# Optimization experiments

Measured on AMD Instinct MI355X. Metric: run time of the kernel, lower is better.

The kernel has to match this reference:

```python
import jax, jax.numpy as jnp
import numpy as np

B, NIMG, H, W, C = 4, 4, 80, 80, 256
NH = 8
C1 = C // 8          # 32
CPH = C1 // NH       # 4 per-head conv channels
K2D = 4              # deformable attention sampling points
HD2 = C1 // NH       # 4 head dim for 2D deformable attention
INNER = 32           # 3D deformable attention inner dim
DSF = (2, 8, 8)
OSC = jnp.array([2.0, 8.0, 8.0], jnp.float32)


def _bilin2d(img, px, py):
    # img [B,C,H,W]; px,py [B,K] pixel coords -> [B,K,C], zero-padded outside
    Bb, Cc, Hh, Ww = img.shape
    x0 = jnp.floor(px); y0 = jnp.floor(py)
    wx = px - x0; wy = py - y0
    bidx = jnp.arange(Bb)[:, None]
    def g(yy, xx):
        valid = (xx >= 0) & (xx <= Ww - 1) & (yy >= 0) & (yy <= Hh - 1)
        xi = jnp.clip(xx, 0, Ww - 1).astype(jnp.int32)
        yi = jnp.clip(yy, 0, Hh - 1).astype(jnp.int32)
        return img[bidx, :, yi, xi] * valid[..., None]
    return (g(y0, x0) * ((1 - wy) * (1 - wx))[..., None]
          + g(y0, x0 + 1) * ((1 - wy) * wx)[..., None]
          + g(y0 + 1, x0) * (wy * (1 - wx))[..., None]
          + g(y0 + 1, x0 + 1) * (wy * wx)[..., None])


def _trilin(img, z, y, x):
    # img [B,C,D,H,W]; z,y,x [B,K] -> [B,K,C]
    Bb, Cc, Dd, Hh, Ww = img.shape
    z0 = jnp.floor(z); y0 = jnp.floor(y); x0 = jnp.floor(x)
    wz = z - z0; wy = y - y0; wx = x - x0
    bidx = jnp.arange(Bb)[:, None]
    def g(zz, yy, xx):
        valid = (zz >= 0) & (zz <= Dd - 1) & (yy >= 0) & (yy <= Hh - 1) & (xx >= 0) & (xx <= Ww - 1)
        zi = jnp.clip(zz, 0, Dd - 1).astype(jnp.int32)
        yi = jnp.clip(yy, 0, Hh - 1).astype(jnp.int32)
        xi = jnp.clip(xx, 0, Ww - 1).astype(jnp.int32)
        return img[bidx, :, zi, yi, xi] * valid[..., None]
    out = 0.
    for dz in (0., 1.):
        for dy in (0., 1.):
            for dx in (0., 1.):
                w = ((1 - wz) if dz == 0. else wz) * ((1 - wy) if dy == 0. else wy) * ((1 - wx) if dx == 0. else wx)
                out = out + g(z0 + dz, y0 + dy, x0 + dx) * w[..., None]
    return out


def _fwd(x, W_qkv, b_qkv, W_fc, b_fc, W_doff, b_doff, W_dep, b_dep, W_st, b_st,
         W_off2d, b_off2d, W_attw, b_attw, W_val, b_val, W_out2d, b_out2d,
         W_q3, b_q3, W_k3, b_k3, W_v3, b_v3, W_offA, b_offA, W_offB, b_offB,
         W_out3, b_out3, rate1, rate2, nimg):
    xb = jnp.transpose(x, (1, 0, 2))                       # [B, nHW, C]
    Bb = xb.shape[0]
    qkv = xb @ W_qkv + b_qkv                               # [B, nHW, 2*C1]
    # ---------- deformable-conv (ACMix) branch ----------
    f_all = qkv.reshape(Bb, nimg * H * W, 2 * NH, CPH).transpose(0, 2, 1, 3)
    f9 = jnp.einsum('oc,bcnk->bonk', W_fc, f_all) + b_fc[None, :, None, None]
    f_conv = f9.transpose(0, 3, 1, 2).reshape(Bb, 9 * CPH, nimg, H, W)
    fin = f_conv.transpose(0, 2, 1, 3, 4).reshape(Bb * nimg, 9 * CPH, H, W)
    off = jax.lax.conv_general_dilated(fin, W_doff, (1, 1), ((1, 1), (1, 1)),
          dimension_numbers=('NCHW', 'OIHW', 'NCHW')) + b_doff[None, :, None, None]
    off = off.reshape(Bb * nimg, 9, 2, H, W)               # (dy,dx) per 3x3 tap
    hh, ww = jnp.meshgrid(jnp.arange(H, dtype=jnp.float32), jnp.arange(W, dtype=jnp.float32), indexing='ij')
    tap = jnp.arange(9)
    ky = (tap // 3 - 1).astype(jnp.float32); kx = (tap % 3 - 1).astype(jnp.float32)
    py = hh[None, None] + ky[None, :, None, None] + off[:, :, 0]
    px = ww[None, None] + kx[None, :, None, None] + off[:, :, 1]
    samp = _bilin2d(fin, px.reshape(Bb * nimg, -1), py.reshape(Bb * nimg, -1))
    samp = samp.reshape(Bb * nimg, 9, H, W, 9 * CPH).transpose(0, 4, 1, 2, 3)
    sg = samp.reshape(Bb * nimg, CPH, 9, 9, H, W)          # [Bn, g, cin_pg, taps, H, W]
    wg = W_dep.reshape(CPH, 27, 9, 9)                      # [g, out_pg, cin_pg, taps]
    dep = jnp.einsum('bgikhw,goik->bgohw', sg, wg).reshape(Bb * nimg, 27 * CPH, H, W) + b_dep[None, :, None, None]
    oc = dep.reshape(Bb, nimg, 27 * CPH, H, W).transpose(0, 2, 1, 3, 4)
    st_in = oc.reshape(Bb, CPH, 27, nimg, H, W)
    st = jnp.einsum('bginhw,goi->bgonhw', st_in, W_st).reshape(Bb, C, nimg, H, W) + b_st[None, :, None, None, None]
    out_conv = st.transpose(2, 3, 4, 0, 1).reshape(nimg * H * W, Bb, C)
    # ---------- per-frame 2D deformable attention ----------
    qk = qkv.reshape(Bb, nimg, H, W, 2, C1)
    q2 = qk[..., 0, :].reshape(Bb * nimg, H, W, C1)
    k2 = qk[..., 1, :].reshape(Bb * nimg, H, W, C1)
    gy, gx = jnp.meshgrid(jnp.arange(H, dtype=jnp.float32) / (H - 1),
                          jnp.arange(W, dtype=jnp.float32) / (W - 1), indexing='ij')
    ref = jnp.stack([gx, gy], -1)                          # [H,W,2] normalized (x,y)
    off2 = (q2 @ W_off2d + b_off2d).reshape(Bb * nimg, H, W, NH, K2D, 2)
    attw = jax.nn.softmax((q2 @ W_attw + b_attw).reshape(Bb * nimg, H, W, NH, K2D), axis=-1)
    v2 = (k2 @ W_val + b_val).reshape(Bb * nimg, H, W, NH, HD2)
    vimg = v2.transpose(0, 3, 4, 1, 2).reshape(Bb * nimg * NH, HD2, H, W)
    loc = ref[None, :, :, None, None, :] + off2 / jnp.array([W, H], jnp.float32)
    ppx = (loc[..., 0] * (W - 1)).transpose(0, 3, 1, 2, 4).reshape(Bb * nimg * NH, H * W * K2D)
    ppy = (loc[..., 1] * (H - 1)).transpose(0, 3, 1, 2, 4).reshape(Bb * nimg * NH, H * W * K2D)
    s2 = _bilin2d(vimg, ppx, ppy).reshape(Bb * nimg, NH, H, W, K2D, HD2)
    a2 = jnp.einsum('bhwnk,bnhwkd->bhwnd', attw, s2).reshape(Bb * nimg, H, W, C1)
    a2 = (a2 @ W_out2d + b_out2d).reshape(Bb, nimg, H, W, C1)
    # faithful reproduction of the source's frame-concat bug: frames [0,0,1,...,nimg-2]
    idx = jnp.array([0] + list(range(nimg - 1)))
    x3 = a2[:, idx].transpose(0, 4, 1, 2, 3)               # [B, C1, nimg, H, W]
    # ---------- 3D deformable attention ----------
    q3 = jnp.einsum('oc,bcnhw->bonhw', W_q3, x3) + b_q3[None, :, None, None, None]
    hid = jax.lax.conv_general_dilated(q3, W_offA, DSF, ((1, 1), (1, 1), (1, 1)),
          dimension_numbers=('NCDHW', 'OIDHW', 'NCDHW')) + b_offA[None, :, None, None, None]
    hid = jax.nn.gelu(hid)
    off3 = jnp.einsum('oc,bcnhw->bonhw', W_offB, hid) + b_offB[None, :, None, None, None]
    off3 = jnp.tanh(off3) * OSC[None, :, None, None, None]
    npr, hpr, wpr = off3.shape[2], off3.shape[3], off3.shape[4]
    gz, gy2, gx2 = jnp.meshgrid(jnp.arange(npr, dtype=jnp.float32) * 2 + 0.5,
                                jnp.arange(hpr, dtype=jnp.float32) * 8 + 3.5,
                                jnp.arange(wpr, dtype=jnp.float32) * 8 + 3.5, indexing='ij')
    cz = (gz[None] + off3[:, 0]).reshape(Bb, -1)
    cy = (gy2[None] + off3[:, 1]).reshape(Bb, -1)
    cx = (gx2[None] + off3[:, 2]).reshape(Bb, -1)
    kf = jnp.einsum('oc,bcnhw->bonhw', W_k3, x3) + b_k3[None, :, None, None, None]
    vf = jnp.einsum('oc,bcnhw->bonhw', W_v3, x3) + b_v3[None, :, None, None, None]
    ks_ = _trilin(kf, cz, cy, cx)                          # [B, L, INNER]
    vs_ = _trilin(vf, cz, cy, cx)
    qf = q3.reshape(Bb, INNER, -1).transpose(0, 2, 1)      # [B, N, INNER]
    at = jax.nn.softmax(jnp.einsum('bnd,bld->bnl', qf, ks_) * (INNER ** -0.5), axis=-1)
    o3 = jnp.einsum('bnl,bld->bnd', at, vs_).transpose(0, 2, 1).reshape(Bb, INNER, nimg, H, W)
    o3 = jnp.einsum('oc,bcnhw->bonhw', W_out3, o3) + b_out3[None, :, None, None, None]
    xattn = o3.transpose(2, 3, 4, 0, 1).reshape(nimg * H * W, Bb, C)
    return rate1 * xattn + rate2 * out_conv


def _p(key, shape, s=0.02):
    return jax.random.normal(key, shape, jnp.float32) * s


def setup_inputs() -> dict:
    key = jax.random.key(0)
    ks = jax.random.split(key, 20)
    z = lambda *s: jnp.zeros(s, jnp.float32)
    return {
        'x': jax.random.normal(ks[0], (NIMG * H * W, B, C), jnp.float32),
        'W_qkv': _p(ks[1], (C, C // 4)), 'b_qkv': z(C // 4),
        'W_fc': _p(ks[2], (9, 2 * NH)), 'b_fc': z(9),
        'W_doff': _p(ks[3], (18, 9 * CPH, 3, 3), 0.01), 'b_doff': z(18),
        'W_dep': _p(ks[4], (27 * CPH, 9, 3, 3)), 'b_dep': z(27 * CPH),
        'W_st': _p(ks[5], (CPH, C // CPH, 27)), 'b_st': z(C),
        'W_off2d': _p(ks[6], (C1, NH * K2D * 2), 0.01), 'b_off2d': z(NH * K2D * 2),
        'W_attw': _p(ks[7], (C1, NH * K2D)), 'b_attw': z(NH * K2D),
        'W_val': _p(ks[8], (C1, C1)), 'b_val': z(C1),
        'W_out2d': _p(ks[9], (C1, C1)), 'b_out2d': z(C1),
        'W_q3': _p(ks[10], (INNER, C1)), 'b_q3': z(INNER),
        'W_k3': _p(ks[11], (INNER, C1)), 'b_k3': z(INNER),
        'W_v3': _p(ks[12], (INNER, C1)), 'b_v3': z(INNER),
        'W_offA': _p(ks[13], (INNER, INNER, 4, 10, 10), 0.01), 'b_offA': z(INNER),
        'W_offB': _p(ks[14], (3, INNER), 0.01), 'b_offB': z(3),
        'W_out3': _p(ks[15], (C, INNER)), 'b_out3': z(C),
        'rate1': jnp.full((1,), 0.5, jnp.float32),
        'rate2': jnp.full((1,), 0.5, jnp.float32),
        'nimg': NIMG,
    }


def reference(x, W_qkv, b_qkv, W_fc, b_fc, W_doff, b_doff, W_dep, b_dep, W_st, b_st,
              W_off2d, b_off2d, W_attw, b_attw, W_val, b_val, W_out2d, b_out2d,
              W_q3, b_q3, W_k3, b_k3, W_v3, b_v3, W_offA, b_offA, W_offB, b_offB,
              W_out3, b_out3, rate1, rate2, nimg):
    return _fwd(x, W_qkv, b_qkv, W_fc, b_fc, W_doff, b_doff, W_dep, b_dep, W_st, b_st,
                W_off2d, b_off2d, W_attw, b_attw, W_val, b_val, W_out2d, b_out2d,
                W_q3, b_q3, W_k3, b_k3, W_v3, b_v3, W_offA, b_offA, W_offB, b_offB,
                W_out3, b_out3, rate1, rate2, nimg)
```

## Files before the change

### kernel.cpp

```cpp
#include <hip/hip_runtime.h>
#include <math.h>

#define B_     4
#define NIMG_  4
#define H_     80
#define W_     80
#define C_     256
#define NH_    8
#define HW_    6400
#define NQ_    25600
#define NPIX_  102400
#define L3_    200

#define WS_QKV 0u
#define WS_Q3  0u
#define WS_KF  3276800u
#define WS_FIN 6553600u
#define WS_A2  6553600u
#define WS_O3  6553600u
#define WS_OFF 10240000u
#define WS_CRD 10240000u
#define WS_KS  10242400u
#define WS_VS  10268000u
#define WS_V2  12083200u
#define WS_VF  12083200u

__global__ __launch_bounds__(256) void k_qkv(const float* __restrict__ x,
        const float* __restrict__ Wq, const float* __restrict__ bq,
        float* __restrict__ qkv) {
    __shared__ __align__(16) float xs[32][256];
    int t = threadIdx.x;
    int row0 = blockIdx.x * 32;
    for (int it = 0; it < 8; ++it) {
        int idx = t + it * 256;
        int r = idx >> 6;
        int f4 = idx & 63;
        int row = row0 + r;
        int b = row / NQ_, n = row % NQ_;
        const float4* src = (const float4*)(x + ((size_t)n * B_ + b) * C_);
        ((float4*)&xs[r][0])[f4] = src[f4];
    }
    __syncthreads();
    int j = t & 63;
    int rbase = (t >> 6) * 8;
    float acc[8];
    #pragma unroll
    for (int r = 0; r < 8; ++r) acc[r] = 0.f;
    for (int c4 = 0; c4 < 64; ++c4) {
        float w0 = Wq[(c4 * 4 + 0) * 64 + j];
        float w1 = Wq[(c4 * 4 + 1) * 64 + j];
        float w2 = Wq[(c4 * 4 + 2) * 64 + j];
        float w3 = Wq[(c4 * 4 + 3) * 64 + j];
        #pragma unroll
        for (int r = 0; r < 8; ++r) {
            float4 xv = ((const float4*)&xs[rbase + r][0])[c4];
            acc[r] += xv.x * w0 + xv.y * w1 + xv.z * w2 + xv.w * w3;
        }
    }
    float bias = bq[j];
    #pragma unroll
    for (int r = 0; r < 8; ++r) {
        int row = row0 + rbase + r;
        qkv[(size_t)row * 64 + j] = acc[r] + bias;
    }
}

__global__ __launch_bounds__(256) void k_fin_v2(const float* __restrict__ qkv,
        const float* __restrict__ Wfc, const float* __restrict__ bfc,
        const float* __restrict__ Wval, const float* __restrict__ bval,
        float* __restrict__ fin, float* __restrict__ v2) {
    __shared__ float WvalL[1024], WfcL[144], bfcL[9], bvalL[32];
    int t = threadIdx.x;
    for (int d = t; d < 1024; d += 256) WvalL[d] = Wval[d];
    if (t < 144) WfcL[t] = Wfc[t];
    if (t >= 160 && t < 169) bfcL[t - 160] = bfc[t - 160];
    if (t >= 192 && t < 224) bvalL[t - 192] = bval[t - 192];
    __syncthreads();
    int P = blockIdx.x * 256 + t;
    int b = P / NQ_, nq = P % NQ_;
    int n = nq / HW_, hw = nq % HW_;
    int bn = b * NIMG_ + n;
    float q[64];
    const float4* qp = (const float4*)(qkv + (size_t)P * 64);
    #pragma unroll
    for (int i = 0; i < 16; ++i) ((float4*)q)[i] = qp[i];
    float fo[36];
    #pragma unroll
    for (int k = 0; k < 4; ++k)
        #pragma unroll
        for (int o = 0; o < 9; ++o) fo[k * 9 + o] = bfcL[o];
    for (int c = 0; c < 16; ++c) {
        #pragma unroll
        for (int o = 0; o < 9; ++o) {
            float wv = WfcL[o * 16 + c];
            #pragma unroll
            for (int k = 0; k < 4; ++k) fo[k * 9 + o] += wv * q[c * 4 + k];
        }
    }
    float* fp = fin + ((size_t)bn * HW_ + hw) * 36;
    #pragma unroll
    for (int i = 0; i < 9; ++i) ((float4*)fp)[i] = ((float4*)fo)[i];
    float vo[32];
    #pragma unroll
    for (int j = 0; j < 32; ++j) vo[j] = bvalL[j];
    for (int c = 0; c < 32; ++c) {
        float qc = q[32 + c];
        #pragma unroll
        for (int j = 0; j < 32; ++j) vo[j] += qc * WvalL[c * 32 + j];
    }
    float* vp = v2 + ((size_t)bn * HW_ + hw) * 32;
    #pragma unroll
    for (int i = 0; i < 8; ++i) ((float4*)vp)[i] = ((float4*)vo)[i];
}

__global__ __launch_bounds__(256) void k_offconv(const float* __restrict__ fin,
        const float* __restrict__ Wdoff, const float* __restrict__ bdoff,
        float* __restrict__ off) {
    __shared__ float Wl[5832];
    int t = threadIdx.x;
    for (int d = t; d < 5832; d += 256) {
        int tap = d / 648, r = d % 648, c = r / 18, o = r % 18;
        Wl[d] = Wdoff[(o * 36 + c) * 9 + tap];
    }
    __syncthreads();
    int P = blockIdx.x * 256 + t;
    int bn = P / HW_, hw = P % HW_;
    int h = hw / W_, w = hw % W_;
    float acc[18];
    #pragma unroll
    for (int o = 0; o < 18; ++o) acc[o] = bdoff[o];
    for (int ky = 0; ky < 3; ++ky) {
        int hh = h + ky - 1;
        if (hh < 0 || hh >= H_) continue;
        for (int kx = 0; kx < 3; ++kx) {
            int ww = w + kx - 1;
            if (ww < 0 || ww >= W_) continue;
            const float* base = fin + ((size_t)bn * HW_ + hh * W_ + ww) * 36;
            const float* wl = Wl + (ky * 3 + kx) * 648;
            #pragma unroll
            for (int c4 = 0; c4 < 9; ++c4) {
                float4 v = ((const float4*)base)[c4];
                const float* w0 = wl + (c4 * 4) * 18;
                #pragma unroll
                for (int o = 0; o < 18; ++o)
                    acc[o] += v.x * w0[o] + v.y * w0[18 + o] + v.z * w0[36 + o] + v.w * w0[54 + o];
            }
        }
    }
    float* op = off + (size_t)P * 18;
    #pragma unroll
    for (int o = 0; o < 18; ++o) op[o] = acc[o];
}

__global__ __launch_bounds__(512, 4) void k_depst(const float* __restrict__ fin,
        const float* __restrict__ off, const float* __restrict__ Wdep,
        const float* __restrict__ bdep, const float* __restrict__ Wst,
        const float* __restrict__ bst, const float* __restrict__ rate2p,
        float* __restrict__ out) {
    __shared__ __align__(16) float wdepL[9072];
    __shared__ __align__(16) float wstL[6944];
    __shared__ float offL[2304];
    __shared__ float bdepL[108];
    __shared__ float bstL[256];
    int t = threadIdx.x;
    int bx = blockIdx.x;
    int pb = (bx & 7) * 100 + (bx >> 3);
    int P0 = pb * 128;
    for (int d = t; d < 9072; d += 512) {
        int g2 = d / 2268, r = d % 2268;
        int k = r / 252, r2 = r % 252;
        int i = r2 / 28, o = r2 % 28;
        wdepL[d] = (o < 27) ? Wdep[(size_t)(g2 * 27 + o) * 81 + i * 9 + k] : 0.f;
    }
    for (int d = t; d < 6944; d += 512) {
        int g2 = d / 1736, r = d % 1736;
        int i = r >> 6, o = r & 63;
        wstL[d] = (r < 1728) ? Wst[g2 * 1728 + o * 27 + i] : 0.f;
    }
    for (int d = t; d < 2304; d += 512) offL[d] = off[(size_t)P0 * 18 + d];
    if (t < 108) bdepL[t] = bdep[t];
    if (t < 256) bstL[t] = bst[t];
    __syncthreads();
    int g = t & 3, ploc = t >> 2;
    int P = P0 + ploc;
    int bn = P / HW_, hw = P % HW_;
    int h = hw / W_, w = hw % W_;
    int b = bn >> 2, n = bn & 3;
    const float* finb = fin + (size_t)bn * HW_ * 36 + g * 9;
    const float* wdg = wdepL + g * 2268;
    const float* wsg = wstL + g * 1736;
    float acc[27];
    #pragma unroll
    for (int o = 0; o < 27; ++o) acc[o] = 0.f;
    float hf = (float)h, wf = (float)w;
    #pragma unroll 1
    for (int k = 0; k < 9; ++k) {
        float py = hf + (float)(k / 3 - 1) + offL[ploc * 18 + k * 2 + 0];
        float px = wf + (float)(k % 3 - 1) + offL[ploc * 18 + k * 2 + 1];
        float y0f = floorf(py), x0f = floorf(px);
        float wy = py - y0f, wx = px - x0f;
        float wy0 = 1.f - wy, wx0 = 1.f - wx;
        float vy0 = (y0f >= 0.f && y0f <= 79.f) ? 1.f : 0.f;
        float vy1 = (y0f >= -1.f && y0f <= 78.f) ? 1.f : 0.f;
        float vx0 = (x0f >= 0.f && x0f <= 79.f) ? 1.f : 0.f;
        float vx1 = (x0f >= -1.f && x0f <= 78.f) ? 1.f : 0.f;
        int yi0 = (int)fminf(fmaxf(y0f, 0.f), 79.f);
        int yi1 = (int)fminf(fmaxf(y0f + 1.f, 0.f), 79.f);
        int xi0 = (int)fminf(fmaxf(x0f, 0.f), 79.f);
        int xi1 = (int)fminf(fmaxf(x0f + 1.f, 0.f), 79.f);
        float w00 = wy0 * wx0 * vy0 * vx0;
        float w01 = wy0 * wx  * vy0 * vx1;
        float w10 = wy  * wx0 * vy1 * vx0;
        float w11 = wy  * wx  * vy1 * vx1;
        const float* c00 = finb + ((size_t)(yi0 * W_ + xi0)) * 36;
        const float* c01 = finb + ((size_t)(yi0 * W_ + xi1)) * 36;
        const float* c10 = finb + ((size_t)(yi1 * W_ + xi0)) * 36;
        const float* c11 = finb + ((size_t)(yi1 * W_ + xi1)) * 36;
        float s[9];
        #pragma unroll
        for (int i = 0; i < 9; ++i)
            s[i] = w00 * c00[i] + w01 * c01[i] + w10 * c10[i] + w11 * c11[i];
        const float* wk = wdg + k * 252;
        #pragma unroll
        for (int i = 0; i < 9; ++i) {
            float si = s[i];
            const float4* rw = (const float4*)(wk + i * 28);
            float4 q0 = rw[0], q1 = rw[1], q2 = rw[2], q3 = rw[3];
            float4 q4 = rw[4], q5 = rw[5], q6 = rw[6];
            acc[0]  += si * q0.x; acc[1]  += si * q0.y; acc[2]  += si * q0.z; acc[3]  += si * q0.w;
            acc[4]  += si * q1.x; acc[5]  += si * q1.y; acc[6]  += si * q1.z; acc[7]  += si * q1.w;
            acc[8]  += si * q2.x; acc[9]  += si * q2.y; acc[10] += si * q2.z; acc[11] += si * q2.w;
            acc[12] += si * q3.x; acc[13] += si * q3.y; acc[14] += si * q3.z; acc[15] += si * q3.w;
            acc[16] += si * q4.x; acc[17] += si * q4.y; acc[18] += si * q4.z; acc[19] += si * q4.w;
            acc[20] += si * q5.x; acc[21] += si * q5.y; acc[22] += si * q5.z; acc[23] += si * q5.w;
            acc[24] += si * q6.x; acc[25] += si * q6.y; acc[26] += si * q6.z;
        }
    }
    #pragma unroll
    for (int i = 0; i < 27; ++i) acc[i] += bdepL[g * 27 + i];
    float r2v = rate2p[0];
    float* ob = out + ((size_t)(n * HW_ + hw) * B_ + b) * C_ + g * 64;
    #pragma unroll 1
    for (int half = 0; half < 2; ++half) {
        float ro[32];
        #pragma unroll
        for (int o = 0; o < 32; ++o) ro[o] = bstL[g * 64 + half * 32 + o];
        #pragma unroll
        for (int i = 0; i < 27; ++i) {
            float ai = acc[i];
            const float4* rw = (const float4*)(wsg + i * 64 + half * 32);
            #pragma unroll
            for (int j = 0; j < 8; ++j) {
                float4 wv = rw[j];
                ro[j * 4 + 0] += ai * wv.x;
                ro[j * 4 + 1] += ai * wv.y;
                ro[j * 4 + 2] += ai * wv.z;
                ro[j * 4 + 3] += ai * wv.w;
            }
        }
        float4* obv = (float4*)(ob + half * 32);
        #pragma unroll
        for (int o4 = 0; o4 < 8; ++o4)
            obv[o4] = make_float4(r2v * ro[o4 * 4 + 0], r2v * ro[o4 * 4 + 1],
                                  r2v * ro[o4 * 4 + 2], r2v * ro[o4 * 4 + 3]);
    }
}

__global__ __launch_bounds__(256) void k_attn2d(const float* __restrict__ qkv,
        const float* __restrict__ v2,
        const float* __restrict__ Woff, const float* __restrict__ boff,
        const float* __restrict__ Watt, const float* __restrict__ batt,
        const float* __restrict__ Wout, const float* __restrict__ bout,
        float* __restrict__ a2) {
    __shared__ float WoffL[2048], WattL[1024], WoutL[1024];
    __shared__ float boffL[64], battL[32], boutL[32];
    int t = threadIdx.x;
    for (int d = t; d < 2048; d += 256) WoffL[d] = Woff[d];
    for (int d = t; d < 1024; d += 256) { WattL[d] = Watt[d]; WoutL[d] = Wout[d]; }
    if (t < 64) boffL[t] = boff[t];
    else if (t < 96) battL[t - 64] = batt[t - 64];
    else if (t < 128) boutL[t - 96] = bout[t - 96];
    __syncthreads();
    int P = blockIdx.x * 256 + t;
    int b = P / NQ_, nq = P % NQ_;
    int n = nq / HW_, hw = nq % HW_;
    int h = hw / W_, w = hw % W_;
    int bn = b * NIMG_ + n;
    float q[32];
    const float4* qp = (const float4*)(qkv + (size_t)P * 64);
    #pragma unroll
    for (int i = 0; i < 8; ++i) ((float4*)q)[i] = qp[i];
    const float* vbase = v2 + (size_t)bn * HW_ * 32;
    float a2v[32];
    #pragma unroll
    for (int i = 0; i < 32; ++i) a2v[i] = 0.f;
    for (int nh = 0; nh < 8; ++nh) {
        float t0 = battL[nh * 4 + 0], t1 = battL[nh * 4 + 1];
        float t2 = battL[nh * 4 + 2], t3 = battL[nh * 4 + 3];
        for (int c = 0; c < 32; ++c) {
            float qc = q[c];
            const float* wr = WattL + c * 32 + nh * 4;
            t0 += qc * wr[0]; t1 += qc * wr[1]; t2 += qc * wr[2]; t3 += qc * wr[3];
        }
        float m = fmaxf(fmaxf(t0, t1), fmaxf(t2, t3));
        float e0 = expf(t0 - m), e1 = expf(t1 - m), e2 = expf(t2 - m), e3 = expf(t3 - m);
        float inv = 1.f / (e0 + e1 + e2 + e3);
        float pk[4] = {e0 * inv, e1 * inv, e2 * inv, e3 * inv};
        #pragma unroll
        for (int kk = 0; kk < 4; ++kk) {
            int j0 = nh * 8 + kk * 2;
            float ox = boffL[j0], oy = boffL[j0 + 1];
            for (int c = 0; c < 32; ++c) {
                float qc = q[c];
                ox += qc * WoffL[c * 64 + j0];
                oy += qc * WoffL[c * 64 + j0 + 1];
            }
            float ppx = (float)w + ox * (79.f / 80.f);
            float ppy = (float)h + oy * (79.f / 80.f);
            float x0 = floorf(ppx), y0 = floorf(ppy);
            float wx = ppx - x0, wy = ppy - y0;
            float s0 = 0.f, s1 = 0.f, s2 = 0.f, s3 = 0.f;
            #pragma unroll
            for (int cy = 0; cy < 2; ++cy) {
                float yf = y0 + (float)cy;
                if (yf < 0.f || yf > 79.f) continue;
                float wyf = cy ? wy : 1.f - wy;
                int yi = (int)yf;
                #pragma unroll
                for (int cx = 0; cx < 2; ++cx) {
                    float xf = x0 + (float)cx;
                    if (xf < 0.f || xf > 79.f) continue;
                    float wgt = wyf * (cx ? wx : 1.f - wx);
                    int xi = (int)xf;
                    float4 vv = *(const float4*)(vbase + ((size_t)yi * W_ + xi) * 32 + nh * 4);
                    s0 += wgt * vv.x; s1 += wgt * vv.y; s2 += wgt * vv.z; s3 += wgt * vv.w;
                }
            }
            float p = pk[kk];
            a2v[nh * 4 + 0] += p * s0; a2v[nh * 4 + 1] += p * s1;
            a2v[nh * 4 + 2] += p * s2; a2v[nh * 4 + 3] += p * s3;
        }
    }
    float ro[32];
    #pragma unroll
    for (int o = 0; o < 32; ++o) ro[o] = boutL[o];
    for (int c = 0; c < 32; ++c) {
        float ac = a2v[c];
        const float* wr = WoutL + c * 32;
        #pragma unroll
        for (int o = 0; o < 32; ++o) ro[o] += ac * wr[o];
    }
    float* op = a2 + ((size_t)bn * HW_ + hw) * 32;
    #pragma unroll
    for (int i = 0; i < 8; ++i) ((float4*)op)[i] = ((float4*)ro)[i];
}

__global__ __launch_bounds__(256) void k_qkv3(const float* __restrict__ a2,
        const float* __restrict__ Wq3, const float* __restrict__ bq3,
        const float* __restrict__ Wk3, const float* __restrict__ bk3,
        const float* __restrict__ Wv3, const float* __restrict__ bv3,
        float* __restrict__ q3, float* __restrict__ kf, float* __restrict__ vf) {
    __shared__ float Wq3L[1024], Wk3L[1024], Wv3L[1024];
    __shared__ float bq3L[32], bk3L[32], bv3L[32];
    int t = threadIdx.x;
    for (int d = t; d < 1024; d += 256) {
        Wq3L[d] = Wq3[d]; Wk3L[d] = Wk3[d]; Wv3L[d] = Wv3[d];
    }
    if (t < 32) { bq3L[t] = bq3[t]; bk3L[t] = bk3[t]; bv3L[t] = bv3[t]; }
    __syncthreads();
    int idx = blockIdx.x * 256 + t;
    int bn = idx / HW_, hw = idx % HW_;
    int b = bn >> 2, n = bn & 3;
    int ns = (n == 0) ? 0 : n - 1;
    const float* src = a2 + ((size_t)(b * 4 + ns) * HW_ + hw) * 32;
    float v[32];
    #pragma unroll
    for (int i = 0; i < 8; ++i) ((float4*)v)[i] = ((const float4*)src)[i];
    float oq[32], ok[32], ov[32];
    #pragma unroll
    for (int o = 0; o < 32; ++o) {
        float aq = bq3L[o], ak = bk3L[o], av = bv3L[o];
        #pragma unroll
        for (int c = 0; c < 32; ++c) {
            aq += Wq3L[o * 32 + c] * v[c];
            ak += Wk3L[o * 32 + c] * v[c];
            av += Wv3L[o * 32 + c] * v[c];
        }
        oq[o] = aq; ok[o] = ak; ov[o] = av;
    }
    float* qo = q3 + (size_t)idx * 32;
    float* ko = kf + (size_t)idx * 32;
    float* vo = vf + (size_t)idx * 32;
    #pragma unroll
    for (int i = 0; i < 8; ++i) {
        ((float4*)qo)[i] = ((float4*)oq)[i];
        ((float4*)ko)[i] = ((float4*)ok)[i];
        ((float4*)vo)[i] = ((float4*)ov)[i];
    }
}

__global__ __launch_bounds__(256) void k_offs3d(const float* __restrict__ q3,
        const float* __restrict__ WoffA, const float* __restrict__ boffA,
        const float* __restrict__ WoffB, const float* __restrict__ boffB,
        float* __restrict__ coords) {
    __shared__ float red[4][128];
    __shared__ float hidl[128];
    int t = threadIdx.x;
    int blk = blockIdx.x;
    int zo = blk / 100, r = blk % 100, ho = r / 10, wo = r % 10;
    float acc[4][32];
    #pragma unroll
    for (int b = 0; b < 4; ++b)
        #pragma unroll
        for (int o = 0; o < 32; ++o) acc[b][o] = 0.f;
    for (int tap = t; tap < 400; tap += 256) {
        int kz = tap / 100, r2 = tap % 100, ky = r2 / 10, kx = r2 % 10;
        int zi = zo * 2 + kz - 1, hi = ho * 8 + ky - 1, wi = wo * 8 + kx - 1;
        if (zi < 0 || zi >= NIMG_ || hi < 0 || hi >= H_ || wi < 0 || wi >= W_) continue;
        const float* wb = WoffA + tap;
        int sp = hi * W_ + wi;
        for (int c = 0; c < 32; ++c) {
            float vb[4];
            #pragma unroll
            for (int b = 0; b < 4; ++b)
                vb[b] = q3[((size_t)(b * 4 + zi) * HW_ + sp) * 32 + c];
            #pragma unroll
            for (int o = 0; o < 32; ++o) {
                float wv = wb[(o * 32 + c) * 400];
                #pragma unroll
                for (int b = 0; b < 4; ++b) acc[b][o] += vb[b] * wv;
            }
        }
    }
    #pragma unroll
    for (int b = 0; b < 4; ++b)
        #pragma unroll
        for (int o = 0; o < 32; ++o)
            for (int sh = 32; sh >= 1; sh >>= 1)
                acc[b][o] += __shfl_xor(acc[b][o], sh);
    int lane = t & 63, wv = t >> 6;
    if (lane == 0)
        for (int b = 0; b < 4; ++b)
            for (int o = 0; o < 32; ++o) red[wv][b * 32 + o] = acc[b][o];
    __syncthreads();
    if (t < 128) {
        float v = red[0][t] + red[1][t] + red[2][t] + red[3][t] + boffA[t & 31];
        float v3 = v * v * v;
        hidl[t] = 0.5f * v * (1.f + tanhf(0.7978845608028654f * (v + 0.044715f * v3)));
    }
    __syncthreads();
    if (t < 12) {
        int b = t / 3, j = t % 3;
        float a = boffB[j];
        for (int o = 0; o < 32; ++o) a += WoffB[j * 32 + o] * hidl[b * 32 + o];
        float osc = (j == 0) ? 2.f : 8.f;
        float base = (j == 0) ? (zo * 2 + 0.5f) : ((j == 1) ? (ho * 8 + 3.5f) : (wo * 8 + 3.5f));
        coords[((size_t)b * L3_ + blk) * 3 + j] = base + tanhf(a) * osc;
    }
}

__global__ __launch_bounds__(256) void k_trisample(const float* __restrict__ kf,
        const float* __restrict__ vf, const float* __restrict__ coords,
        float* __restrict__ ks, float* __restrict__ vs) {
    int t = threadIdx.x;
    int wv = blockIdx.x * 4 + (t >> 6);
    int b = wv / L3_, l = wv % L3_;
    int lane = t & 63;
    int c = lane & 31;
    const float* src = (lane < 32) ? kf : vf;
    float* dst = (lane < 32) ? ks : vs;
    const float* cp = coords + ((size_t)b * L3_ + l) * 3;
    float cz = cp[0], cy = cp[1], cx = cp[2];
    float z0 = floorf(cz), y0 = floorf(cy), x0 = floorf(cx);
    float wz = cz - z0, wy = cy - y0, wx = cx - x0;
    float acc = 0.f;
    #pragma unroll
    for (int dz = 0; dz < 2; ++dz) {
        float zf = z0 + (float)dz;
        if (zf < 0.f || zf > 3.f) continue;
        float wzf = dz ? wz : 1.f - wz;
        int zi = (int)zf;
        #pragma unroll
        for (int dy = 0; dy < 2; ++dy) {
            float yf = y0 + (float)dy;
            if (yf < 0.f || yf > 79.f) continue;
            float wyf = wzf * (dy ? wy : 1.f - wy);
            int yi = (int)yf;
            #pragma unroll
            for (int dx = 0; dx < 2; ++dx) {
                float xf = x0 + (float)dx;
                if (xf < 0.f || xf > 79.f) continue;
                float wgt = wyf * (dx ? wx : 1.f - wx);
                int xi = (int)xf;
                acc += wgt * src[((size_t)(b * 4 + zi) * HW_ + yi * W_ + xi) * 32 + c];
            }
        }
    }
    dst[((size_t)b * L3_ + l) * 32 + c] = acc;
}

__global__ __launch_bounds__(256) void k_attn3d(const float* __restrict__ q3,
        const float* __restrict__ ks, const float* __restrict__ vs,
        float* __restrict__ o3) {
    __shared__ __align__(16) float ksl[L3_ * 32];
    __shared__ __align__(16) float vsl[L3_ * 32];
    int t = threadIdx.x;
    int b = blockIdx.x / 100;
    int chunk = blockIdx.x % 100;
    const float4* ksg = (const float4*)(ks + (size_t)b * L3_ * 32);
    const float4* vsg = (const float4*)(vs + (size_t)b * L3_ * 32);
    for (int d = t; d < L3_ * 8; d += 256) {
        ((float4*)ksl)[d] = ksg[d];
        ((float4*)vsl)[d] = vsg[d];
    }
    __syncthreads();
    int N = chunk * 256 + t;
    float q[32];
    const float4* qp = (const float4*)(q3 + ((size_t)b * NQ_ + N) * 32);
    #pragma unroll
    for (int i = 0; i < 8; ++i) ((float4*)q)[i] = qp[i];
    const float scale = 0.17677669529663687f;
    float den = 0.f;
    float o[32];
    #pragma unroll
    for (int c = 0; c < 32; ++c) o[c] = 0.f;
    for (int l = 0; l < L3_; ++l) {
        const float4* kp = (const float4*)(ksl + l * 32);
        float s = 0.f;
        #pragma unroll
        for (int c4 = 0; c4 < 8; ++c4) {
            float4 kv = kp[c4];
            s += q[c4 * 4 + 0] * kv.x + q[c4 * 4 + 1] * kv.y + q[c4 * 4 + 2] * kv.z + q[c4 * 4 + 3] * kv.w;
        }
        float p = expf(s * scale);
        den += p;
        const float4* vp = (const float4*)(vsl + l * 32);
        #pragma unroll
        for (int c4 = 0; c4 < 8; ++c4) {
            float4 vv = vp[c4];
            o[c4 * 4 + 0] += p * vv.x; o[c4 * 4 + 1] += p * vv.y;
            o[c4 * 4 + 2] += p * vv.z; o[c4 * 4 + 3] += p * vv.w;
        }
    }
    float inv = 1.f / den;
    float* op = o3 + ((size_t)b * NQ_ + N) * 32;
    #pragma unroll
    for (int c = 0; c < 32; ++c) op[c] = o[c] * inv;
}

__global__ __launch_bounds__(256) void k_final(const float* __restrict__ o3,
        const float* __restrict__ W, const float* __restrict__ bias,
        const float* __restrict__ r1p, float* __restrict__ out) {
    __shared__ float o3T[32 * 128];
    __shared__ float WT[32 * 260];
    int t = threadIdx.x;
    int R0 = blockIdx.x * 128;
    {
        int row = t >> 1, k0 = (t & 1) * 16;
        int R = R0 + row;
        int b = R & 3, N = R >> 2;
        const float* src = o3 + ((size_t)b * NQ_ + N) * 32 + k0;
        #pragma unroll
        for (int j = 0; j < 16; ++j) o3T[(k0 + j) * 128 + row] = src[j];
    }
    for (int d = t; d < 8192; d += 256) {
        int c = d >> 5, k = d & 31;
        WT[k * 260 + c] = W[d];
    }
    __syncthreads();
    int tc = t & 15;
    int tr = t >> 4;
    int r0 = tr * 8;
    float acc[8][16];
    #pragma unroll
    for (int i = 0; i < 8; ++i)
        #pragma unroll
        for (int j = 0; j < 16; ++j) acc[i][j] = 0.f;
    #pragma unroll 1
    for (int k = 0; k < 32; ++k) {
        float a[8];
        *(float4*)&a[0] = *(const float4*)&o3T[k * 128 + r0];
        *(float4*)&a[4] = *(const float4*)&o3T[k * 128 + r0 + 4];
        float wv[16];
        #pragma unroll
        for (int ci = 0; ci < 16; ++ci) wv[ci] = WT[k * 260 + tc + 16 * ci];
        #pragma unroll
        for (int i = 0; i < 8; ++i)
            #pragma unroll
            for (int j = 0; j < 16; ++j) acc[i][j] += a[i] * wv[j];
    }
    float r1 = r1p[0];
    float bs[16];
    #pragma unroll
    for (int ci = 0; ci < 16; ++ci) bs[ci] = bias[tc + 16 * ci];
    #pragma unroll 1
    for (int i = 0; i < 8; ++i) {
        size_t rowbase = (size_t)(R0 + r0 + i) * 256;
        #pragma unroll
        for (int j = 0; j < 16; ++j) {
            size_t oi = rowbase + tc + 16 * j;
            out[oi] = r1 * (acc[i][j] + bs[j]) + out[oi];
        }
    }
}

extern "C" void kernel_launch(void* const* d_in, const int* in_sizes, int n_in,
                              void* d_out, int out_size, void* d_ws, size_t ws_size,
                              hipStream_t stream) {
    (void)in_sizes; (void)n_in; (void)out_size; (void)ws_size;
    const float* x      = (const float*)d_in[0];
    const float* W_qkv  = (const float*)d_in[1];
    const float* b_qkv  = (const float*)d_in[2];
    const float* W_fc   = (const float*)d_in[3];
    const float* b_fc   = (const float*)d_in[4];
    const float* W_doff = (const float*)d_in[5];
    const float* b_doff = (const float*)d_in[6];
    const float* W_dep  = (const float*)d_in[7];
    const float* b_dep  = (const float*)d_in[8];
    const float* W_st   = (const float*)d_in[9];
    const float* b_st   = (const float*)d_in[10];
    const float* W_off2d= (const float*)d_in[11];
    const float* b_off2d= (const float*)d_in[12];
    const float* W_attw = (const float*)d_in[13];
    const float* b_attw = (const float*)d_in[14];
    const float* W_val  = (const float*)d_in[15];
    const float* b_val  = (const float*)d_in[16];
    const float* W_out2d= (const float*)d_in[17];
    const float* b_out2d= (const float*)d_in[18];
    const float* W_q3   = (const float*)d_in[19];
    const float* b_q3   = (const float*)d_in[20];
    const float* W_k3   = (const float*)d_in[21];
    const float* b_k3   = (const float*)d_in[22];
    const float* W_v3   = (const float*)d_in[23];
    const float* b_v3   = (const float*)d_in[24];
    const float* W_offA = (const float*)d_in[25];
    const float* b_offA = (const float*)d_in[26];
    const float* W_offB = (const float*)d_in[27];
    const float* b_offB = (const float*)d_in[28];
    const float* W_out3 = (const float*)d_in[29];
    const float* b_out3 = (const float*)d_in[30];
    const float* rate1  = (const float*)d_in[31];
    const float* rate2  = (const float*)d_in[32];

    float* ws  = (float*)d_ws;
    float* out = (float*)d_out;
    float* qkv = ws + WS_QKV;
    float* fin = ws + WS_FIN;
    float* off = ws + WS_OFF;
    float* v2  = ws + WS_V2;
    float* a2  = ws + WS_A2;
    float* q3  = ws + WS_Q3;
    float* kf  = ws + WS_KF;
    float* vf  = ws + WS_VF;
    float* crd = ws + WS_CRD;
    float* ks  = ws + WS_KS;
    float* vs  = ws + WS_VS;
    float* o3w = ws + WS_O3;

    k_qkv      <<<3200,   256, 0, stream>>>(x, W_qkv, b_qkv, qkv);
    k_fin_v2   <<<400,    256, 0, stream>>>(qkv, W_fc, b_fc, W_val, b_val, fin, v2);
    k_offconv  <<<400,    256, 0, stream>>>(fin, W_doff, b_doff, off);
    k_depst    <<<800,    512, 0, stream>>>(fin, off, W_dep, b_dep, W_st, b_st, rate2, out);
    k_attn2d   <<<400,    256, 0, stream>>>(qkv, v2, W_off2d, b_off2d, W_attw, b_attw, W_out2d, b_out2d, a2);
    k_qkv3     <<<400,    256, 0, stream>>>(a2, W_q3, b_q3, W_k3, b_k3, W_v3, b_v3, q3, kf, vf);
    k_offs3d   <<<200,    256, 0, stream>>>(q3, W_offA, b_offA, W_offB, b_offB, crd);
    k_trisample<<<200,    256, 0, stream>>>(kf, vf, crd, ks, vs);
    k_attn3d   <<<400,    256, 0, stream>>>(q3, ks, vs, o3w);
    k_final    <<<800,    256, 0, stream>>>(o3w, W_out3, b_out3, rate1, out);
}
```

Measured before the change: 918.2 us.

## Split fin into per-group padded planes and give each depst block one group

The 36-channel fin buffer becomes four group-major planes, each holding 9 values per pixel padded to 12. The deformable-conv kernel now gives one group per block of 256 threads, so each block loads only that group's weights into LDS, which shrinks shared memory and raises occupancy. Offsets are now read straight from global memory instead of being staged in LDS, and bilinear taps use aligned float4 loads. The qkv output is split into separate q and k buffers and the workspace layout is reshuffled, at the cost of more padded bytes and a different access pattern in offconv.

```diff
diff --git a/kernel.cpp b/kernel.cpp
--- a/kernel.cpp
+++ b/kernel.cpp
@@ -12,22 +12,23 @@
 #define NPIX_  102400
 #define L3_    200
 
-#define WS_QKV 0u
-#define WS_Q3  0u
-#define WS_KF  3276800u
-#define WS_FIN 6553600u
-#define WS_A2  6553600u
-#define WS_O3  6553600u
-#define WS_OFF 10240000u
-#define WS_CRD 10240000u
-#define WS_KS  10242400u
-#define WS_VS  10268000u
-#define WS_V2  12083200u
-#define WS_VF  12083200u
+#define WS_QH   0u
+#define WS_KH   3276800u
+#define WS_V2   6553600u
+#define WS_FING 9830400u
+#define WS_OFF  3276800u
+#define WS_A2   9830400u
+#define WS_Q3   0u
+#define WS_KF   3276800u
+#define WS_VF   6553600u
+#define WS_CRD  9830400u
+#define WS_KS   9832800u
+#define WS_VS   9858400u
+#define WS_O3   3276800u
 
 __global__ __launch_bounds__(256) void k_qkv(const float* __restrict__ x,
         const float* __restrict__ Wq, const float* __restrict__ bq,
-        float* __restrict__ qkv) {
+        float* __restrict__ qh, float* __restrict__ kh) {
     __shared__ __align__(16) float xs[32][256];
     int t = threadIdx.x;
     int row0 = blockIdx.x * 32;
@@ -61,14 +62,17 @@
     #pragma unroll
     for (int r = 0; r < 8; ++r) {
         int row = row0 + rbase + r;
-        qkv[(size_t)row * 64 + j] = acc[r] + bias;
-    }
-}
-
-__global__ __launch_bounds__(256) void k_fin_v2(const float* __restrict__ qkv,
+        float vres = acc[r] + bias;
+        if (j < 32) qh[(size_t)row * 32 + j] = vres;
+        else        kh[(size_t)row * 32 + (j - 32)] = vres;
+    }
+}
+
+__global__ __launch_bounds__(256) void k_fin_v2(const float* __restrict__ qh,
+        const float* __restrict__ kh,
         const float* __restrict__ Wfc, const float* __restrict__ bfc,
         const float* __restrict__ Wval, const float* __restrict__ bval,
-        float* __restrict__ fin, float* __restrict__ v2) {
+        float* __restrict__ fing, float* __restrict__ v2) {
     __shared__ float WvalL[1024], WfcL[144], bfcL[9], bvalL[32];
     int t = threadIdx.x;
     for (int d = t; d < 1024; d += 256) WvalL[d] = Wval[d];
@@ -81,9 +85,12 @@
     int n = nq / HW_, hw = nq % HW_;
     int bn = b * NIMG_ + n;
     float q[64];
-    const float4* qp = (const float4*)(qkv + (size_t)P * 64);
-    #pragma unroll
-    for (int i = 0; i < 16; ++i) ((float4*)q)[i] = qp[i];
+    const float4* qp = (const float4*)(qh + (size_t)P * 32);
+    const float4* kp = (const float4*)(kh + (size_t)P * 32);
+    #pragma unroll
+    for (int i = 0; i < 8; ++i) ((float4*)q)[i] = qp[i];
+    #pragma unroll
+    for (int i = 0; i < 8; ++i) ((float4*)q)[8 + i] = kp[i];
     float fo[36];
     #pragma unroll
     for (int k = 0; k < 4; ++k)
@@ -97,9 +104,13 @@
             for (int k = 0; k < 4; ++k) fo[k * 9 + o] += wv * q[c * 4 + k];
         }
     }
-    float* fp = fin + ((size_t)bn * HW_ + hw) * 36;
-    #pragma unroll
-    for (int i = 0; i < 9; ++i) ((float4*)fp)[i] = ((float4*)fo)[i];
+    #pragma unroll
+    for (int g = 0; g < 4; ++g) {
+        float* fp = fing + ((size_t)(g * 16 + bn) * HW_ + hw) * 12;
+        ((float4*)fp)[0] = make_float4(fo[g * 9 + 0], fo[g * 9 + 1], fo[g * 9 + 2], fo[g * 9 + 3]);
+        ((float4*)fp)[1] = make_float4(fo[g * 9 + 4], fo[g * 9 + 5], fo[g * 9 + 6], fo[g * 9 + 7]);
+        ((float4*)fp)[2] = make_float4(fo[g * 9 + 8], 0.f, 0.f, 0.f);
+    }
     float vo[32];
     #pragma unroll
     for (int j = 0; j < 32; ++j) vo[j] = bvalL[j];
@@ -113,7 +124,7 @@
     for (int i = 0; i < 8; ++i) ((float4*)vp)[i] = ((float4*)vo)[i];
 }
 
-__global__ __launch_bounds__(256) void k_offconv(const float* __restrict__ fin,
+__global__ __launch_bounds__(256) void k_offconv(const float* __restrict__ fing,
         const float* __restrict__ Wdoff, const float* __restrict__ bdoff,
         float* __restrict__ off) {
     __shared__ float Wl[5832];
@@ -135,15 +146,21 @@
         for (int kx = 0; kx < 3; ++kx) {
             int ww = w + kx - 1;
             if (ww < 0 || ww >= W_) continue;
-            const float* base = fin + ((size_t)bn * HW_ + hh * W_ + ww) * 36;
+            int sp = hh * W_ + ww;
             const float* wl = Wl + (ky * 3 + kx) * 648;
             #pragma unroll
-            for (int c4 = 0; c4 < 9; ++c4) {
-                float4 v = ((const float4*)base)[c4];
-                const float* w0 = wl + (c4 * 4) * 18;
+            for (int g = 0; g < 4; ++g) {
+                const float4* base = (const float4*)(fing
+                        + ((size_t)(g * 16 + bn) * HW_ + sp) * 12);
+                float4 p0 = base[0], p1 = base[1], p2 = base[2];
+                float vals[9] = {p0.x, p0.y, p0.z, p0.w, p1.x, p1.y, p1.z, p1.w, p2.x};
                 #pragma unroll
-                for (int o = 0; o < 18; ++o)
-                    acc[o] += v.x * w0[o] + v.y * w0[18 + o] + v.z * w0[36 + o] + v.w * w0[54 + o];
+                for (int idx = 0; idx < 9; ++idx) {
+                    const float* w0 = wl + (g * 9 + idx) * 18;
+                    float vv = vals[idx];
+                    #pragma unroll
+                    for (int o = 0; o < 18; ++o) acc[o] += vv * w0[o];
+                }
             }
         }
     }
@@ -152,51 +169,46 @@
     for (int o = 0; o < 18; ++o) op[o] = acc[o];
 }
 
-__global__ __launch_bounds__(512, 4) void k_depst(const float* __restrict__ fin,
+__global__ __launch_bounds__(256, 6) void k_depst(const float* __restrict__ fing,
         const float* __restrict__ off, const float* __restrict__ Wdep,
         const float* __restrict__ bdep, const float* __restrict__ Wst,
         const float* __restrict__ bst, const float* __restrict__ rate2p,
         float* __restrict__ out) {
-    __shared__ __align__(16) float wdepL[9072];
-    __shared__ __align__(16) float wstL[6944];
-    __shared__ float offL[2304];
-    __shared__ float bdepL[108];
-    __shared__ float bstL[256];
+    __shared__ __align__(16) float wdepL[2268];
+    __shared__ __align__(16) float wstL[1728];
+    __shared__ float bdepL[27];
+    __shared__ float bstL[64];
     int t = threadIdx.x;
     int bx = blockIdx.x;
-    int pb = (bx & 7) * 100 + (bx >> 3);
-    int P0 = pb * 128;
-    for (int d = t; d < 9072; d += 512) {
-        int g2 = d / 2268, r = d % 2268;
-        int k = r / 252, r2 = r % 252;
+    int u = (bx & 7) * 200 + (bx >> 3);
+    int chunk = u >> 2, g = u & 3;
+    for (int d = t; d < 2268; d += 256) {
+        int k = d / 252, r2 = d % 252;
         int i = r2 / 28, o = r2 % 28;
-        wdepL[d] = (o < 27) ? Wdep[(size_t)(g2 * 27 + o) * 81 + i * 9 + k] : 0.f;
-    }
-    for (int d = t; d < 6944; d += 512) {
-        int g2 = d / 1736, r = d % 1736;
-        int i = r >> 6, o = r & 63;
-        wstL[d] = (r < 1728) ? Wst[g2 * 1728 + o * 27 + i] : 0.f;
-    }
-    for (int d = t; d < 2304; d += 512) offL[d] = off[(size_t)P0 * 18 + d];
-    if (t < 108) bdepL[t] = bdep[t];
-    if (t < 256) bstL[t] = bst[t];
-    __syncthreads();
-    int g = t & 3, ploc = t >> 2;
-    int P = P0 + ploc;
+        wdepL[d] = (o < 27) ? Wdep[(size_t)(g * 27 + o) * 81 + i * 9 + k] : 0.f;
+    }
+    for (int d = t; d < 1728; d += 256) {
+        int i = d >> 6, o = d & 63;
+        wstL[d] = Wst[g * 1728 + o * 27 + i];
+    }
+    if (t < 27) bdepL[t] = bdep[g * 27 + t];
+    if (t >= 32 && t < 96) bstL[t - 32] = bst[g * 64 + (t - 32)];
+    __syncthreads();
+    int P = chunk * 256 + t;
     int bn = P / HW_, hw = P % HW_;
     int h = hw / W_, w = hw % W_;
     int b = bn >> 2, n = bn & 3;
-    const float* finb = fin + (size_t)bn * HW_ * 36 + g * 9;
-    const float* wdg = wdepL + g * 2268;
-    const float* wsg = wstL + g * 1736;
+    const float* finb = fing + (size_t)(g * 16 + bn) * (HW_ * 12);
+    const float* offp = off + (size_t)P * 18;
     float acc[27];
     #pragma unroll
     for (int o = 0; o < 27; ++o) acc[o] = 0.f;
     float hf = (float)h, wf = (float)w;
     #pragma unroll 1
     for (int k = 0; k < 9; ++k) {
-        float py = hf + (float)(k / 3 - 1) + offL[ploc * 18 + k * 2 + 0];
-        float px = wf + (float)(k % 3 - 1) + offL[ploc * 18 + k * 2 + 1];
+        float2 od = *(const float2*)(offp + k * 2);
+        float py = hf + (float)(k / 3 - 1) + od.x;
+        float px = wf + (float)(k % 3 - 1) + od.y;
         float y0f = floorf(py), x0f = floorf(px);
         float wy = py - y0f, wx = px - x0f;
         float wy0 = 1.f - wy, wx0 = 1.f - wx;
@@ -212,43 +224,64 @@
         float w01 = wy0 * wx  * vy0 * vx1;
         float w10 = wy  * wx0 * vy1 * vx0;
         float w11 = wy  * wx  * vy1 * vx1;
-        const float* c00 = finb + ((size_t)(yi0 * W_ + xi0)) * 36;
-        const float* c01 = finb + ((size_t)(yi0 * W_ + xi1)) * 36;
-        const float* c10 = finb + ((size_t)(yi1 * W_ + xi0)) * 36;
-        const float* c11 = finb + ((size_t)(yi1 * W_ + xi1)) * 36;
+        const float4* c00 = (const float4*)(finb + (size_t)(yi0 * W_ + xi0) * 12);
+        const float4* c01 = (const float4*)(finb + (size_t)(yi0 * W_ + xi1) * 12);
+        const float4* c10 = (const float4*)(finb + (size_t)(yi1 * W_ + xi0) * 12);
+        const float4* c11 = (const float4*)(finb + (size_t)(yi1 * W_ + xi1) * 12);
         float s[9];
-        #pragma unroll
-        for (int i = 0; i < 9; ++i)
-            s[i] = w00 * c00[i] + w01 * c01[i] + w10 * c10[i] + w11 * c11[i];
-        const float* wk = wdg + k * 252;
+        {
+            float4 p0 = c00[0], p1 = c00[1], p2 = c00[2];
+            s[0] = w00 * p0.x; s[1] = w00 * p0.y; s[2] = w00 * p0.z; s[3] = w00 * p0.w;
+            s[4] = w00 * p1.x; s[5] = w00 * p1.y; s[6] = w00 * p1.z; s[7] = w00 * p1.w;
+            s[8] = w00 * p2.x;
+        }
+        {
+            float4 p0 = c01[0], p1 = c01[1], p2 = c01[2];
+            s[0] += w01 * p0.x; s[1] += w01 * p0.y; s[2] += w01 * p0.z; s[3] += w01 * p0.w;
+            s[4] += w01 * p1.x; s[5] += w01 * p1.y; s[6] += w01 * p1.z; s[7] += w01 * p1.w;
+            s[8] += w01 * p2.x;
+        }
+        {
+            float4 p0 = c10[0], p1 = c10[1], p2 = c10[2];
+            s[0] += w10 * p0.x; s[1] += w10 * p0.y; s[2] += w10 * p0.z; s[3] += w10 * p0.w;
+            s[4] += w10 * p1.x; s[5] += w10 * p1.y; s[6] += w10 * p1.z; s[7] += w10 * p1.w;
+            s[8] += w10 * p2.x;
+        }
+        {
+            float4 p0 = c11[0], p1 = c11[1], p2 = c11[2];
+            s[0] += w11 * p0.x; s[1] += w11 * p0.y; s[2] += w11 * p0.z; s[3] += w11 * p0.w;
+            s[4] += w11 * p1.x; s[5] += w11 * p1.y; s[6] += w11 * p1.z; s[7] += w11 * p1.w;
+            s[8] += w11 * p2.x;
+        }
+        const float* wk = wdepL + k * 252;
         #pragma unroll
         for (int i = 0; i < 9; ++i) {
             float si = s[i];
             const float4* rw = (const float4*)(wk + i * 28);
-            float4 q0 = rw[0], q1 = rw[1], q2 = rw[2], q3 = rw[3];
+            float4 q0 = rw[0], q1 = rw[1], q2 = rw[2], q3v = rw[3];
             float4 q4 = rw[4], q5 = rw[5], q6 = rw[6];
-            acc[0]  += si * q0.x; acc[1]  += si * q0.y; acc[2]  += si * q0.z; acc[3]  += si * q0.w;
-            acc[4]  += si * q1.x; acc[5]  += si * q1.y; acc[6]  += si * q1.z; acc[7]  += si * q1.w;
-            acc[8]  += si * q2.x; acc[9]  += si * q2.y; acc[10] += si * q2.z; acc[11] += si * q2.w;
-            acc[12] += si * q3.x; acc[13] += si * q3.y; acc[14] += si * q3.z; acc[15] += si * q3.w;
-            acc[16] += si * q4.x; acc[17] += si * q4.y; acc[18] += si * q4.z; acc[19] += si * q4.w;
-            acc[20] += si * q5.x; acc[21] += si * q5.y; acc[22] += si * q5.z; acc[23] += si * q5.w;
-            acc[24] += si * q6.x; acc[25] += si * q6.y; acc[26] += si * q6.z;
-        }
-    }
-    #pragma unroll
-    for (int i = 0; i < 27; ++i) acc[i] += bdepL[g * 27 + i];
+            acc[0]  += si * q0.x;  acc[1]  += si * q0.y;  acc[2]  += si * q0.z;  acc[3]  += si * q0.w;
+            acc[4]  += si * q1.x;  acc[5]  += si * q1.y;  acc[6]  += si * q1.z;  acc[7]  += si * q1.w;
+            acc[8]  += si * q2.x;  acc[9]  += si * q2.y;  acc[10] += si * q2.z;  acc[11] += si * q2.w;
+            acc[12] += si * q3v.x; acc[13] += si * q3v.y; acc[14] += si * q3v.z; acc[15] += si * q3v.w;
+            acc[16] += si * q4.x;  acc[17] += si * q4.y;  acc[18] += si * q4.z;  acc[19] += si * q4.w;
+            acc[20] += si * q5.x;  acc[21] += si * q5.y;  acc[22] += si * q5.z;  acc[23] += si * q5.w;
+            acc[24] += si * q6.x;  acc[25] += si * q6.y;  acc[26] += si * q6.z;
+        }
+    }
+    #pragma unroll
+    for (int i = 0; i < 27; ++i) acc[i] += bdepL[i];
     float r2v = rate2p[0];
     float* ob = out + ((size_t)(n * HW_ + hw) * B_ + b) * C_ + g * 64;
     #pragma unroll 1
     for (int half = 0; half < 2; ++half) {
         float ro[32];
         #pragma unroll
-        for (int o = 0; o < 32; ++o) ro[o] = bstL[g * 64 + half * 32 + o];
+        for (int o = 0; o < 32; ++o) ro[o] = bstL[half * 32 + o];
         #pragma unroll
         for (int i = 0; i < 27; ++i) {
             float ai = acc[i];
-            const float4* rw = (const float4*)(wsg + i * 64 + half * 32);
+            const float4* rw = (const float4*)(wstL + i * 64 + half * 32);
             #pragma unroll
             for (int j = 0; j < 8; ++j) {
                 float4 wv = rw[j];
@@ -266,7 +299,7 @@
     }
 }
 
-__global__ __launch_bounds__(256) void k_attn2d(const float* __restrict__ qkv,
+__global__ __launch_bounds__(256) void k_attn2d(const float* __restrict__ qh,
         const float* __restrict__ v2,
         const float* __restrict__ Woff, const float* __restrict__ boff,
         const float* __restrict__ Watt, const float* __restrict__ batt,
@@ -287,7 +320,7 @@
     int h = hw / W_, w = hw % W_;
     int bn = b * NIMG_ + n;
     float q[32];
-    const float4* qp = (const float4*)(qkv + (size_t)P * 64);
+    const float4* qp = (const float4*)(qh + (size_t)P * 32);
     #pragma unroll
     for (int i = 0; i < 8; ++i) ((float4*)q)[i] = qp[i];
     const float* vbase = v2 + (size_t)bn * HW_ * 32;
@@ -644,8 +677,9 @@
 
     float* ws  = (float*)d_ws;
     float* out = (float*)d_out;
-    float* qkv = ws + WS_QKV;
-    float* fin = ws + WS_FIN;
+    float* qhp = ws + WS_QH;
+    float* khp = ws + WS_KH;
+    float* fng = ws + WS_FING;
     float* off = ws + WS_OFF;
     float* v2  = ws + WS_V2;
     float* a2  = ws + WS_A2;
@@ -657,11 +691,11 @@
     float* vs  = ws + WS_VS;
     float* o3w = ws + WS_O3;
 
-    k_qkv      <<<3200,   256, 0, stream>>>(x, W_qkv, b_qkv, qkv);
-    k_fin_v2   <<<400,    256, 0, stream>>>(qkv, W_fc, b_fc, W_val, b_val, fin, v2);
-    k_offconv  <<<400,    256, 0, stream>>>(fin, W_doff, b_doff, off);
-    k_depst    <<<800,    512, 0, stream>>>(fin, off, W_dep, b_dep, W_st, b_st, rate2, out);
-    k_attn2d   <<<400,    256, 0, stream>>>(qkv, v2, W_off2d, b_off2d, W_attw, b_attw, W_out2d, b_out2d, a2);
+    k_qkv      <<<3200,   256, 0, stream>>>(x, W_qkv, b_qkv, qhp, khp);
+    k_fin_v2   <<<400,    256, 0, stream>>>(qhp, khp, W_fc, b_fc, W_val, b_val, fng, v2);
+    k_offconv  <<<400,    256, 0, stream>>>(fng, W_doff, b_doff, off);
+    k_depst    <<<1600,   256, 0, stream>>>(fng, off, W_dep, b_dep, W_st, b_st, rate2, out);
+    k_attn2d   <<<400,    256, 0, stream>>>(qhp, v2, W_off2d, b_off2d, W_attw, b_attw, W_out2d, b_out2d, a2);
     k_qkv3     <<<400,    256, 0, stream>>>(a2, W_q3, b_q3, W_k3, b_k3, W_v3, b_v3, q3, kf, vf);
     k_offs3d   <<<200,    256, 0, stream>>>(q3, W_offA, b_offA, W_offB, b_offB, crd);
     k_trisample<<<200,    256, 0, stream>>>(kf, vf, crd, ks, vs);
```

Measured after the change: 1.053 ms. 1.15x slower.
